# Performance work log

Measured on AMD Instinct MI355X. Metric: run time of the kernel, lower is better.

Reference implementation:

```python
import jax, jax.numpy as jnp
import numpy as np


def setup_inputs() -> dict:
    key = jax.random.key(0)
    ks = jax.random.split(key, 6)
    C, C8, W, H, B = 512, 64, 64, 64, 4
    x = jax.random.normal(ks[0], (B, C, W, H), dtype=jnp.float32)
    Wf = jax.random.normal(ks[1], (C8, C), dtype=jnp.float32) * (1.0 / np.sqrt(C))
    Wg = jax.random.normal(ks[2], (C8, C), dtype=jnp.float32) * (1.0 / np.sqrt(C))
    Wh = jax.random.normal(ks[3], (C8, C), dtype=jnp.float32) * (1.0 / np.sqrt(C))
    Wv = jax.random.normal(ks[4], (C, C8), dtype=jnp.float32) * (1.0 / np.sqrt(C8))
    gamma = jax.random.normal(ks[5], (1,), dtype=jnp.float32)
    return {"x": x, "Wf": Wf, "Wg": Wg, "Wh": Wh, "Wv": Wv, "gamma": gamma}


def reference(x, Wf, Wg, Wh, Wv, gamma):
    b, c, w, h = x.shape
    n = w * h
    xf = x.reshape(b, c, n)                       # [b, c, n]
    # 1x1 convs == channel-mixing GEMMs
    f = jnp.einsum('oc,bcn->bon', Wf, xf)         # [b, c8, n]
    g = jnp.einsum('oc,bcn->bon', Wg, xf)         # [b, c8, n]
    hmap = jnp.einsum('oc,bcn->bon', Wh, xf)      # [b, c8, n]
    # attn_map[b, i, j] = sum_c f[b, c, i] * g[b, c, j]  (f permuted as in torch)
    attn = jnp.einsum('bci,bcj->bij', f, g)       # [b, n, n]
    # unconventional softmax over dim=1 (rows / the i axis)
    attn = jax.nn.softmax(attn, axis=1)
    sa = jnp.einsum('bcn,bnj->bcj', hmap, attn)   # [b, c8, n]
    sa = sa.reshape(b, -1, w, h)                  # [b, c8, w, h]
    sa = jnp.einsum('oc,bcwh->bowh', Wv, sa)      # [b, c, w, h]
    out = sa * gamma[0] + x
    return out, sa
```

## Files before the change

### kernel.cpp

```cpp
#include <hip/hip_runtime.h>
#include <cstddef>

#define BB 4
#define CC 512
#define NN 4096

using half8  = __attribute__((ext_vector_type(8))) _Float16;
using fp16x2 = __attribute__((ext_vector_type(2))) __fp16;
using short8 = __attribute__((ext_vector_type(8))) short;
using us8    = __attribute__((ext_vector_type(8))) unsigned short;
using f32x4  = __attribute__((ext_vector_type(4))) float;

__device__ __forceinline__ unsigned short f2bf(float x) {
    unsigned int u = __float_as_uint(x);
    u += 0x7fffu + ((u >> 16) & 1u);
    return (unsigned short)(u >> 16);
}

__global__ __launch_bounds__(256) void prep_kernel(
    const float* __restrict__ Wf, const float* __restrict__ Wg,
    const float* __restrict__ Wh, const float* __restrict__ Wv,
    _Float16* __restrict__ Wc16, _Float16* __restrict__ Wv16)
{
    int idx = blockIdx.x * 256 + threadIdx.x;
    int stride = gridDim.x * 256;
    const int N1 = 192 * 512, N2 = 512 * 64;
    for (int i = idx; i < N1 + N2; i += stride) {
        if (i < N1) {
            int row = i >> 9, c = i & 511;
            const float* src = (row < 64) ? Wf : ((row < 128) ? Wg : Wh);
            float sc = (row >= 64 && row < 128) ? 1.4426950408889634f : 1.0f;
            Wc16[i] = (_Float16)(sc * src[(row & 63) * 512 + c]);
        } else {
            int k = i - N1;
            Wv16[k] = (_Float16)Wv[k];
        }
    }
}

__global__ __launch_bounds__(256) void proj_kernel(
    const float* __restrict__ x, const _Float16* __restrict__ Wc16,
    _Float16* __restrict__ Kf, _Float16* __restrict__ Qf,
    unsigned short* __restrict__ Vt)
{
    __shared__ float xsT[2][32][68];
    const int t    = threadIdx.x;
    const int w    = t >> 6;
    const int lane = t & 63;
    const int lh   = lane & 15;
    const int qd   = lane >> 4;
    const int b    = blockIdx.x >> 7;
    const int i0   = (blockIdx.x & 127) << 5;

    f32x4 acc[3][2];
    #pragma unroll
    for (int ot = 0; ot < 3; ot++)
        #pragma unroll
        for (int it = 0; it < 2; it++) { acc[ot][it][0]=0.f; acc[ot][it][1]=0.f; acc[ot][it][2]=0.f; acc[ot][it][3]=0.f; }

    const int ti8 = t & 7;
    const int tc2 = t >> 3;
    const float* xbase = x + (size_t)b*CC*NN + i0 + ti8*4;
    const _Float16* wbase = Wc16 + (size_t)(w*48 + lh)*512 + qd*8;

    float4 st0, st1;
    half8  wcur[2][3], wnxt[2][3];

#define LOADX(ck) do {                                                        \
    st0 = *(const float4*)(xbase + (size_t)((ck)*64 + tc2)*NN);               \
    st1 = *(const float4*)(xbase + (size_t)((ck)*64 + 32 + tc2)*NN);          \
} while (0)
#define STOREX(p_) do {                                                       \
    xsT[p_][ti8*4+0][tc2]    = st0.x; xsT[p_][ti8*4+1][tc2]    = st0.y;       \
    xsT[p_][ti8*4+2][tc2]    = st0.z; xsT[p_][ti8*4+3][tc2]    = st0.w;       \
    xsT[p_][ti8*4+0][32+tc2] = st1.x; xsT[p_][ti8*4+1][32+tc2] = st1.y;       \
    xsT[p_][ti8*4+2][32+tc2] = st1.z; xsT[p_][ti8*4+3][32+tc2] = st1.w;       \
} while (0)
#define LOADW(ck, WD) do {                                                    \
    _Pragma("unroll")                                                         \
    for (int ks_ = 0; ks_ < 2; ks_++)                                         \
        _Pragma("unroll")                                                     \
        for (int ot_ = 0; ot_ < 3; ot_++)                                     \
            WD[ks_][ot_] = *(const half8*)(wbase + (size_t)(ot_*16)*512 + (ck)*64 + ks_*32); \
} while (0)

    LOADX(0); STOREX(0);
    LOADW(0, wcur);
    __syncthreads();

    #pragma unroll
    for (int ck = 0; ck < 8; ck++) {
        const int p = ck & 1;
        if (ck < 7) { LOADX(ck + 1); LOADW(ck + 1, wnxt); }

        #pragma unroll
        for (int ks = 0; ks < 2; ks++) {
            half8 xf[2];
            #pragma unroll
            for (int it = 0; it < 2; it++) {
                const float* xr = &xsT[p][it*16 + lh][ks*32 + qd*8];
                f32x4 xa = *(const f32x4*)xr;
                f32x4 xb = *(const f32x4*)(xr + 4);
                union { fp16x2 h2[4]; half8 h8; } u;
                u.h2[0] = __builtin_amdgcn_cvt_pkrtz(xa[0], xa[1]);
                u.h2[1] = __builtin_amdgcn_cvt_pkrtz(xa[2], xa[3]);
                u.h2[2] = __builtin_amdgcn_cvt_pkrtz(xb[0], xb[1]);
                u.h2[3] = __builtin_amdgcn_cvt_pkrtz(xb[2], xb[3]);
                xf[it] = u.h8;
            }
            #pragma unroll
            for (int ot = 0; ot < 3; ot++)
                #pragma unroll
                for (int it = 0; it < 2; it++)
                    acc[ot][it] = __builtin_amdgcn_mfma_f32_16x16x32_f16(wcur[ks][ot], xf[it], acc[ot][it], 0, 0, 0);
        }

        if (ck < 7) {
            STOREX(p ^ 1);
            #pragma unroll
            for (int ks_ = 0; ks_ < 2; ks_++)
                #pragma unroll
                for (int ot_ = 0; ot_ < 3; ot_++)
                    wcur[ks_][ot_] = wnxt[ks_][ot_];
        }
        __syncthreads();
    }
#undef LOADX
#undef STOREX
#undef LOADW

    #pragma unroll
    for (int ot = 0; ot < 3; ot++) {
        int g16 = w*3 + ot;
        int m   = g16 >> 2;
        int obase = (g16 & 3)*16 + qd*4;
        #pragma unroll
        for (int it = 0; it < 2; it++) {
            int ig = i0 + it*16 + lh;
            #pragma unroll
            for (int r = 0; r < 4; r++) {
                float v = acc[ot][it][r];
                int ol = obase + r;
                if (m == 0)       Kf[((size_t)b*NN + ig)*64 + ol] = (_Float16)v;
                else if (m == 1)  Qf[((size_t)b*NN + ig)*64 + ol] = (_Float16)v;
                else              Vt[((size_t)b*64 + ol)*NN + ig] = f2bf(v);
            }
        }
    }
}

__global__ __launch_bounds__(256) void attn_kernel(
    const _Float16* __restrict__ Kf, const _Float16* __restrict__ Qf,
    const unsigned short* __restrict__ Vt,
    _Float16* __restrict__ Po16, float* __restrict__ Pl)
{
    __shared__ __align__(16) unsigned short Kbuf[128*64];
    __shared__ __align__(16) unsigned short Vbuf[64*128];
    __shared__ __align__(16) unsigned short Psh[4][16*64];

    const int t    = threadIdx.x;
    const int wv   = t >> 6;
    const int lane = t & 63;
    const int lh   = lane & 15;
    const int qd   = lane >> 4;

    const int B   = blockIdx.x;
    const int xcd = B & 7;
    const int rr  = B >> 3;
    const int b   = xcd >> 1;
    const int jt  = (rr & 31)*2 + (xcd & 1);
    const int s   = rr >> 5;
    const int j0  = (jt << 6) + wv*16;

    const unsigned short* Kfu = (const unsigned short*)Kf;

    half8 qf0, qf1;
    {
        const size_t qb = ((size_t)b*NN + j0 + lh)*64 + qd*8;
        qf0 = *(const half8*)(Qf + qb);
        qf1 = *(const half8*)(Qf + qb + 32);
    }

    f32x4 o_acc[4];
    float l_r[4];
    #pragma unroll
    for (int dt = 0; dt < 4; dt++) { o_acc[dt][0]=0.f; o_acc[dt][1]=0.f; o_acc[dt][2]=0.f; o_acc[dt][3]=0.f; }
    #pragma unroll
    for (int r = 0; r < 4; r++) l_r[r] = 0.f;

    const int koff = s*1024;
    const int ki = t >> 3, kc = t & 7;
    const int vd = t >> 4, vc = t & 15;

#define LOADC(ck) do {                                                        \
    size_t kg = ((size_t)b*NN + koff + (ck)*128)*64;                          \
    size_t vg = (size_t)b*64*NN + koff + (ck)*128;                            \
    _Pragma("unroll")                                                         \
    for (int r_ = 0; r_ < 4; r_++) {                                          \
        kst[r_] = *(const us8*)(Kfu + kg + (size_t)(r_*32 + ki)*64 + kc*8);   \
        vst[r_] = *(const us8*)(Vt  + vg + (size_t)(r_*16 + vd)*NN + vc*8);   \
    } } while (0)

#define STOREC() do {                                                         \
    _Pragma("unroll")                                                         \
    for (int r_ = 0; r_ < 4; r_++) {                                          \
        int i_ = r_*32 + ki;                                                  \
        int d_ = r_*16 + vd;                                                  \
        *(us8*)(&Kbuf[i_*64  + ((kc ^ (i_ & 7))*8)])  = kst[r_];              \
        *(us8*)(&Vbuf[d_*128 + ((vc ^ (d_ & 15))*8)]) = vst[r_];              \
    } } while (0)

    us8 kst[4], vst[4];
    LOADC(0);
    STOREC();
    __syncthreads();

    for (int ck = 0; ck < 8; ck++) {
        if (ck < 7) LOADC(ck + 1);

        #pragma unroll
        for (int half = 0; half < 2; half++) {
            const unsigned short* Kb = &Kbuf[half*64*64];
            const unsigned short* Vb = &Vbuf[0];

            f32x4 sc[4];
            #pragma unroll
            for (int it = 0; it < 4; it++) {
                sc[it][0]=0.f; sc[it][1]=0.f; sc[it][2]=0.f; sc[it][3]=0.f;
                const unsigned short* kr = Kb + (it*16 + lh)*64;
                half8 k0 = *(const half8*)(kr + ((qd     ^ (lh & 7))*8));
                half8 k1 = *(const half8*)(kr + (((4+qd) ^ (lh & 7))*8));
                sc[it] = __builtin_amdgcn_mfma_f32_16x16x32_f16(qf0, k0, sc[it], 0,0,0);
                sc[it] = __builtin_amdgcn_mfma_f32_16x16x32_f16(qf1, k1, sc[it], 0,0,0);
            }

            #pragma unroll
            for (int it = 0; it < 4; it++)
                #pragma unroll
                for (int r = 0; r < 4; r++) {
                    float p_ = exp2f(sc[it][r]);
                    l_r[r] += p_;
                    int i_ = it*16 + lh;
                    int j_ = qd*4 + r;
                    Psh[wv][j_*64 + (((i_>>3) ^ (j_ & 7))*8) + (i_ & 7)] = f2bf(p_);
                }
            asm volatile("s_waitcnt lgkmcnt(0)" ::: "memory");

            short8 pf0 = *(const short8*)&Psh[wv][lh*64 + ((qd     ^ (lh & 7))*8)];
            short8 pf1 = *(const short8*)&Psh[wv][lh*64 + (((4+qd) ^ (lh & 7))*8)];

            #pragma unroll
            for (int dt = 0; dt < 4; dt++) {
                const unsigned short* vr = Vb + (dt*16 + lh)*128;
                short8 v0 = *(const short8*)(vr + (((half*8 + qd    ) ^ lh)*8));
                short8 v1 = *(const short8*)(vr + (((half*8 + 4 + qd) ^ lh)*8));
                o_acc[dt] = __builtin_amdgcn_mfma_f32_16x16x32_bf16(pf0, v0, o_acc[dt], 0,0,0);
                o_acc[dt] = __builtin_amdgcn_mfma_f32_16x16x32_bf16(pf1, v1, o_acc[dt], 0,0,0);
            }
        }

        __syncthreads();
        if (ck < 7) STOREC();
        __syncthreads();
    }
#undef LOADC
#undef STOREC

    float inv[4];
    #pragma unroll
    for (int r = 0; r < 4; r++) {
        float l = l_r[r];
        #pragma unroll
        for (int off = 1; off < 16; off <<= 1)
            l += __shfl_xor(l, off);
        l_r[r] = l;
        inv[r] = 1.0f / l;
    }
    const size_t pbase = ((size_t)(s*4 + b)*NN + j0);
    #pragma unroll
    for (int dt = 0; dt < 4; dt++)
        #pragma unroll
        for (int r = 0; r < 4; r++)
            Po16[(pbase + qd*4 + r)*64 + dt*16 + lh] = (_Float16)(o_acc[dt][r] * inv[r]);
    if (lh == 0) {
        #pragma unroll
        for (int r = 0; r < 4; r++)
            Pl[pbase + qd*4 + r] = l_r[r];
    }
}

__global__ __launch_bounds__(256) void outproj_kernel(
    const _Float16* __restrict__ Po16, const float* __restrict__ Pl,
    const _Float16* __restrict__ Wv16,
    const float* __restrict__ x, const float* __restrict__ gamma,
    float* __restrict__ out1, float* __restrict__ out2)
{
    __shared__ float Osh[4][16][36];
    const int t    = threadIdx.x;
    const int w    = t >> 6;
    const int lane = t & 63;
    const int lh   = lane & 15;
    const int qd   = lane >> 4;
    const int b    = blockIdx.x >> 7;
    const int j0   = (blockIdx.x & 127) << 5;
    const float g  = gamma[0];

    half8 sb[2][2];
    #pragma unroll
    for (int jt2 = 0; jt2 < 2; jt2++) {
        const int j = j0 + jt2*16 + lh;
        float os[16];
        #pragma unroll
        for (int k = 0; k < 16; k++) os[k] = 0.f;
        float lsum = 0.f;
        #pragma unroll
        for (int s = 0; s < 4; s++) {
            size_t base = ((size_t)(s*4 + b)*NN + j);
            half8 v0 = *(const half8*)(Po16 + base*64 + qd*8);
            half8 v1 = *(const half8*)(Po16 + base*64 + qd*8 + 32);
            float l = Pl[base];
            #pragma unroll
            for (int k = 0; k < 8; k++) {
                os[k]   = fmaf(l, (float)v0[k], os[k]);
                os[8+k] = fmaf(l, (float)v1[k], os[8+k]);
            }
            lsum += l;
        }
        float inv = 1.0f / lsum;
        union { fp16x2 h2[4]; half8 h8; } u0, u1;
        #pragma unroll
        for (int k = 0; k < 4; k++) {
            u0.h2[k] = __builtin_amdgcn_cvt_pkrtz(os[2*k]*inv,   os[2*k+1]*inv);
            u1.h2[k] = __builtin_amdgcn_cvt_pkrtz(os[8+2*k]*inv, os[8+2*k+1]*inv);
        }
        sb[jt2][0] = u0.h8;
        sb[jt2][1] = u1.h8;
    }

    const int o_loc8 = lane >> 3;
    const int j4     = (lane & 7) * 4;

    #pragma unroll 2
    for (int ot8 = 0; ot8 < 8; ot8++) {
        const int ot = w*8 + ot8;
        const size_t wbase = (size_t)(ot*16 + lh)*64 + qd*8;
        half8 a0 = *(const half8*)(Wv16 + wbase);
        half8 a1 = *(const half8*)(Wv16 + wbase + 32);

        f32x4 acc[2];
        #pragma unroll
        for (int jt2 = 0; jt2 < 2; jt2++) {
            acc[jt2][0]=0.f; acc[jt2][1]=0.f; acc[jt2][2]=0.f; acc[jt2][3]=0.f;
            acc[jt2] = __builtin_amdgcn_mfma_f32_16x16x32_f16(a0, sb[jt2][0], acc[jt2], 0, 0, 0);
            acc[jt2] = __builtin_amdgcn_mfma_f32_16x16x32_f16(a1, sb[jt2][1], acc[jt2], 0, 0, 0);
        }

        #pragma unroll
        for (int jt2 = 0; jt2 < 2; jt2++)
            #pragma unroll
            for (int r = 0; r < 4; r++)
                Osh[w][qd*4 + r][jt2*16 + lh] = acc[jt2][r];
        asm volatile("s_waitcnt lgkmcnt(0)" ::: "memory");

        #pragma unroll
        for (int rr2 = 0; rr2 < 2; rr2++) {
            const int o_loc = o_loc8 + 8*rr2;
            f32x4 v = *(const f32x4*)&Osh[w][o_loc][j4];
            const int o  = ot*16 + o_loc;
            const size_t idx = ((size_t)b*CC + o)*NN + j0 + j4;
            f32x4 xv = *(const f32x4*)(x + idx);
            *(f32x4*)(out2 + idx) = v;
            f32x4 r1;
            r1[0] = fmaf(g, v[0], xv[0]); r1[1] = fmaf(g, v[1], xv[1]);
            r1[2] = fmaf(g, v[2], xv[2]); r1[3] = fmaf(g, v[3], xv[3]);
            *(f32x4*)(out1 + idx) = r1;
        }
        asm volatile("s_waitcnt lgkmcnt(0)" ::: "memory");
    }
}

extern "C" void kernel_launch(void* const* d_in, const int* in_sizes, int n_in,
                              void* d_out, int out_size, void* d_ws, size_t ws_size,
                              hipStream_t stream) {
    const float* x     = (const float*)d_in[0];
    const float* Wf    = (const float*)d_in[1];
    const float* Wg    = (const float*)d_in[2];
    const float* Wh    = (const float*)d_in[3];
    const float* Wv    = (const float*)d_in[4];
    const float* gamma = (const float*)d_in[5];

    float* out1 = (float*)d_out;
    float* out2 = out1 + (size_t)BB*CC*NN;

    const size_t BND = (size_t)BB*NN*64;
    char* wp = (char*)d_ws;
    _Float16*       Kf   = (_Float16*)wp;        wp += BND*2;
    _Float16*       Qf   = (_Float16*)wp;        wp += BND*2;
    unsigned short* Vt   = (unsigned short*)wp;  wp += BND*2;
    _Float16*       Po16 = (_Float16*)wp;        wp += BND*4*2;
    float*          Pl   = (float*)wp;           wp += (size_t)4*BB*NN*4;
    _Float16*       Wc16 = (_Float16*)wp;        wp += (size_t)192*512*2;
    _Float16*       Wv16 = (_Float16*)wp;

    prep_kernel<<<dim3(64), dim3(256), 0, stream>>>(Wf, Wg, Wh, Wv, Wc16, Wv16);
    proj_kernel<<<dim3(BB*128), dim3(256), 0, stream>>>(x, Wc16, Kf, Qf, Vt);
    attn_kernel<<<dim3(BB*256), dim3(256), 0, stream>>>(Kf, Qf, Vt, Po16, Pl);
    outproj_kernel<<<dim3(512), dim3(256), 0, stream>>>(Po16, Pl, Wv16, x, gamma, out1, out2);
}
```

Baseline: 173.5 us.

## Rewrite attention with 32x32 MFMA, register-resident P, async LDS loads

The attention kernel moves from 16x16x32 to 32x32x16 MFMA tiles, with 128 query columns per block and 32 per wave. The probability tile is converted to bf16 and rearranged in registers with permlane32 swaps instead of a round trip through shared memory. K and V chunks are staged with global_load_lds into double-buffered LDS, which drops the register staging and one barrier per chunk. The key-split count becomes a template parameter and uses 8 when the workspace allows, at the cost of more partial outputs for the output projection to merge.

```diff
diff --git a/kernel.cpp b/kernel.cpp
--- a/kernel.cpp
+++ b/kernel.cpp
@@ -10,6 +10,7 @@
 using short8 = __attribute__((ext_vector_type(8))) short;
 using us8    = __attribute__((ext_vector_type(8))) unsigned short;
 using f32x4  = __attribute__((ext_vector_type(4))) float;
+using f32x16 = __attribute__((ext_vector_type(16))) float;
 
 __device__ __forceinline__ unsigned short f2bf(float x) {
     unsigned int u = __float_as_uint(x);
@@ -149,146 +150,142 @@
     }
 }
 
-__global__ __launch_bounds__(256) void attn_kernel(
+template<int SPLITS>
+__global__ __launch_bounds__(256, 3) void attn_kernel(
     const _Float16* __restrict__ Kf, const _Float16* __restrict__ Qf,
     const unsigned short* __restrict__ Vt,
     _Float16* __restrict__ Po16, float* __restrict__ Pl)
 {
-    __shared__ __align__(16) unsigned short Kbuf[128*64];
-    __shared__ __align__(16) unsigned short Vbuf[64*128];
-    __shared__ __align__(16) unsigned short Psh[4][16*64];
+    static_assert(NN % SPLITS == 0, "split");
+    constexpr int KS  = NN / SPLITS;
+    constexpr int NCH = KS / 64;
+
+    __shared__ __align__(16) unsigned short Kb2[2][64*64];
+    __shared__ __align__(16) unsigned short Vb2[2][64*64];
 
     const int t    = threadIdx.x;
     const int wv   = t >> 6;
     const int lane = t & 63;
-    const int lh   = lane & 15;
-    const int qd   = lane >> 4;
-
-    const int B   = blockIdx.x;
-    const int xcd = B & 7;
-    const int rr  = B >> 3;
-    const int b   = xcd >> 1;
-    const int jt  = (rr & 31)*2 + (xcd & 1);
-    const int s   = rr >> 5;
-    const int j0  = (jt << 6) + wv*16;
-
-    const unsigned short* Kfu = (const unsigned short*)Kf;
-
-    half8 qf0, qf1;
+    const int il   = lane & 31;
+    const int h    = lane >> 5;
+
+    const int p  = blockIdx.x;
+    const int v  = (p & 7) * (SPLITS * 16) + (p >> 3);
+    const int jt = v & 31;
+    const int bs = v >> 5;
+    const int b  = bs / SPLITS;
+    const int s  = bs % SPLITS;
+    const int j0w  = jt*128 + wv*32;
+    const int koff = s * KS;
+
+    half8 qfr[4];
     {
-        const size_t qb = ((size_t)b*NN + j0 + lh)*64 + qd*8;
-        qf0 = *(const half8*)(Qf + qb);
-        qf1 = *(const half8*)(Qf + qb + 32);
-    }
-
-    f32x4 o_acc[4];
-    float l_r[4];
-    #pragma unroll
-    for (int dt = 0; dt < 4; dt++) { o_acc[dt][0]=0.f; o_acc[dt][1]=0.f; o_acc[dt][2]=0.f; o_acc[dt][3]=0.f; }
-    #pragma unroll
-    for (int r = 0; r < 4; r++) l_r[r] = 0.f;
-
-    const int koff = s*1024;
-    const int ki = t >> 3, kc = t & 7;
-    const int vd = t >> 4, vc = t & 15;
-
-#define LOADC(ck) do {                                                        \
-    size_t kg = ((size_t)b*NN + koff + (ck)*128)*64;                          \
-    size_t vg = (size_t)b*64*NN + koff + (ck)*128;                            \
-    _Pragma("unroll")                                                         \
-    for (int r_ = 0; r_ < 4; r_++) {                                          \
-        kst[r_] = *(const us8*)(Kfu + kg + (size_t)(r_*32 + ki)*64 + kc*8);   \
-        vst[r_] = *(const us8*)(Vt  + vg + (size_t)(r_*16 + vd)*NN + vc*8);   \
+        const _Float16* qp = Qf + ((size_t)b*NN + j0w + il)*64 + h*8;
+        #pragma unroll
+        for (int sl = 0; sl < 4; sl++) qfr[sl] = *(const half8*)(qp + sl*16);
+    }
+
+    f32x16 o_acc[2];
+    #pragma unroll
+    for (int dt = 0; dt < 2; dt++)
+        #pragma unroll
+        for (int r = 0; r < 16; r++) o_acc[dt][r] = 0.f;
+    float l4[4] = {0.f, 0.f, 0.f, 0.f};
+
+#define STAGE(ck, pb) do {                                                          \
+    const size_t bi_ = (size_t)koff + (size_t)(ck)*64;                              \
+    _Pragma("unroll")                                                               \
+    for (int r_ = 0; r_ < 2; r_++) {                                                \
+        const int slot_ = r_*256 + t;                                               \
+        const int ik_ = slot_ >> 3, c8_ = slot_ & 7;                                \
+        const int sw_ = (c8_ ^ (ik_ & 7)) << 3;                                     \
+        const _Float16* gk_ = Kf + ((size_t)b*NN + bi_ + ik_)*64 + sw_;             \
+        __builtin_amdgcn_global_load_lds(                                           \
+            (const __attribute__((address_space(1))) void*)gk_,                     \
+            (__attribute__((address_space(3))) void*)&Kb2[pb][(r_*256 + wv*64)*8],  \
+            16, 0, 0);                                                              \
+        const unsigned short* gv_ = Vt + ((size_t)b*64 + ik_)*NN + bi_ + sw_;       \
+        __builtin_amdgcn_global_load_lds(                                           \
+            (const __attribute__((address_space(1))) void*)gv_,                     \
+            (__attribute__((address_space(3))) void*)&Vb2[pb][(r_*256 + wv*64)*8],  \
+            16, 0, 0);                                                              \
     } } while (0)
 
-#define STOREC() do {                                                         \
-    _Pragma("unroll")                                                         \
-    for (int r_ = 0; r_ < 4; r_++) {                                          \
-        int i_ = r_*32 + ki;                                                  \
-        int d_ = r_*16 + vd;                                                  \
-        *(us8*)(&Kbuf[i_*64  + ((kc ^ (i_ & 7))*8)])  = kst[r_];              \
-        *(us8*)(&Vbuf[d_*128 + ((vc ^ (d_ & 15))*8)]) = vst[r_];              \
-    } } while (0)
-
-    us8 kst[4], vst[4];
-    LOADC(0);
-    STOREC();
+    STAGE(0, 0);
     __syncthreads();
 
-    for (int ck = 0; ck < 8; ck++) {
-        if (ck < 7) LOADC(ck + 1);
-
-        #pragma unroll
-        for (int half = 0; half < 2; half++) {
-            const unsigned short* Kb = &Kbuf[half*64*64];
-            const unsigned short* Vb = &Vbuf[0];
-
-            f32x4 sc[4];
-            #pragma unroll
-            for (int it = 0; it < 4; it++) {
-                sc[it][0]=0.f; sc[it][1]=0.f; sc[it][2]=0.f; sc[it][3]=0.f;
-                const unsigned short* kr = Kb + (it*16 + lh)*64;
-                half8 k0 = *(const half8*)(kr + ((qd     ^ (lh & 7))*8));
-                half8 k1 = *(const half8*)(kr + (((4+qd) ^ (lh & 7))*8));
-                sc[it] = __builtin_amdgcn_mfma_f32_16x16x32_f16(qf0, k0, sc[it], 0,0,0);
-                sc[it] = __builtin_amdgcn_mfma_f32_16x16x32_f16(qf1, k1, sc[it], 0,0,0);
+    for (int ck = 0; ck < NCH; ck++) {
+        const int cb = ck & 1;
+        if (ck + 1 < NCH) STAGE(ck + 1, cb ^ 1);
+
+        const unsigned short* Kb = Kb2[cb];
+        const unsigned short* Vb = Vb2[cb];
+
+        #pragma unroll
+        for (int isub = 0; isub < 2; isub++) {
+            const int irow = isub*32 + il;
+            const unsigned short* kr = Kb + irow*64;
+            f32x16 sc;
+            #pragma unroll
+            for (int r = 0; r < 16; r++) sc[r] = 0.f;
+            #pragma unroll
+            for (int sl = 0; sl < 4; sl++) {
+                half8 kf = *(const half8*)(kr + (((sl*2 + h) ^ (irow & 7)) << 3));
+                sc = __builtin_amdgcn_mfma_f32_32x32x16_f16(kf, qfr[sl], sc, 0, 0, 0);
             }
 
-            #pragma unroll
-            for (int it = 0; it < 4; it++)
+            float pq[16];
+            #pragma unroll
+            for (int r = 0; r < 16; r++) pq[r] = exp2f(sc[r]);
+            #pragma unroll
+            for (int r = 0; r < 16; r++) l4[r & 3] += pq[r];
+
+            unsigned wA[8];
+            #pragma unroll
+            for (int k = 0; k < 8; k++)
+                asm("v_cvt_pk_bf16_f32 %0, %1, %2" : "=v"(wA[k]) : "v"(pq[2*k]), "v"(pq[2*k+1]));
+            asm("v_permlane32_swap_b32 %0, %1" : "+v"(wA[0]), "+v"(wA[2]));
+            asm("v_permlane32_swap_b32 %0, %1" : "+v"(wA[1]), "+v"(wA[3]));
+            asm("v_permlane32_swap_b32 %0, %1" : "+v"(wA[4]), "+v"(wA[6]));
+            asm("v_permlane32_swap_b32 %0, %1" : "+v"(wA[5]), "+v"(wA[7]));
+
+            union { unsigned u[4]; short8 s8; } pa0, pa1;
+            pa0.u[0]=wA[0]; pa0.u[1]=wA[1]; pa0.u[2]=wA[2]; pa0.u[3]=wA[3];
+            pa1.u[0]=wA[4]; pa1.u[1]=wA[5]; pa1.u[2]=wA[6]; pa1.u[3]=wA[7];
+
+            #pragma unroll
+            for (int isl = 0; isl < 2; isl++) {
+                const short8 paf = isl ? pa1.s8 : pa0.s8;
+                const int vc = isub*4 + isl*2 + h;
                 #pragma unroll
-                for (int r = 0; r < 4; r++) {
-                    float p_ = exp2f(sc[it][r]);
-                    l_r[r] += p_;
-                    int i_ = it*16 + lh;
-                    int j_ = qd*4 + r;
-                    Psh[wv][j_*64 + (((i_>>3) ^ (j_ & 7))*8) + (i_ & 7)] = f2bf(p_);
+                for (int dt = 0; dt < 2; dt++) {
+                    const int drow = dt*32 + il;
+                    short8 vf = *(const short8*)(Vb + drow*64 + ((vc ^ (drow & 7)) << 3));
+                    o_acc[dt] = __builtin_amdgcn_mfma_f32_32x32x16_bf16(paf, vf, o_acc[dt], 0, 0, 0);
                 }
-            asm volatile("s_waitcnt lgkmcnt(0)" ::: "memory");
-
-            short8 pf0 = *(const short8*)&Psh[wv][lh*64 + ((qd     ^ (lh & 7))*8)];
-            short8 pf1 = *(const short8*)&Psh[wv][lh*64 + (((4+qd) ^ (lh & 7))*8)];
-
-            #pragma unroll
-            for (int dt = 0; dt < 4; dt++) {
-                const unsigned short* vr = Vb + (dt*16 + lh)*128;
-                short8 v0 = *(const short8*)(vr + (((half*8 + qd    ) ^ lh)*8));
-                short8 v1 = *(const short8*)(vr + (((half*8 + 4 + qd) ^ lh)*8));
-                o_acc[dt] = __builtin_amdgcn_mfma_f32_16x16x32_bf16(pf0, v0, o_acc[dt], 0,0,0);
-                o_acc[dt] = __builtin_amdgcn_mfma_f32_16x16x32_bf16(pf1, v1, o_acc[dt], 0,0,0);
             }
         }
-
         __syncthreads();
-        if (ck < 7) STOREC();
-        __syncthreads();
-    }
-#undef LOADC
-#undef STOREC
-
-    float inv[4];
-    #pragma unroll
-    for (int r = 0; r < 4; r++) {
-        float l = l_r[r];
-        #pragma unroll
-        for (int off = 1; off < 16; off <<= 1)
-            l += __shfl_xor(l, off);
-        l_r[r] = l;
-        inv[r] = 1.0f / l;
-    }
-    const size_t pbase = ((size_t)(s*4 + b)*NN + j0);
-    #pragma unroll
-    for (int dt = 0; dt < 4; dt++)
-        #pragma unroll
-        for (int r = 0; r < 4; r++)
-            Po16[(pbase + qd*4 + r)*64 + dt*16 + lh] = (_Float16)(o_acc[dt][r] * inv[r]);
-    if (lh == 0) {
-        #pragma unroll
-        for (int r = 0; r < 4; r++)
-            Pl[pbase + qd*4 + r] = l_r[r];
-    }
-}
-
+    }
+#undef STAGE
+
+    float l_acc  = (l4[0] + l4[1]) + (l4[2] + l4[3]);
+    float l_full = l_acc + __shfl_xor(l_acc, 32);
+    float inv = 1.0f / l_full;
+
+    const size_t pbase = (size_t)(s*4 + b)*NN + j0w;
+    #pragma unroll
+    for (int r = 0; r < 16; r++) {
+        const int jr = (r & 3) + 8*(r >> 2) + 4*h;
+        const float invr = __shfl(inv, jr);
+        #pragma unroll
+        for (int dt = 0; dt < 2; dt++)
+            Po16[(pbase + jr)*64 + dt*32 + il] = (_Float16)(o_acc[dt][r] * invr);
+    }
+    if (h == 0) Pl[pbase + il] = l_full;
+}
+
+template<int SPLITS>
 __global__ __launch_bounds__(256) void outproj_kernel(
     const _Float16* __restrict__ Po16, const float* __restrict__ Pl,
     const _Float16* __restrict__ Wv16,
@@ -314,7 +311,7 @@
         for (int k = 0; k < 16; k++) os[k] = 0.f;
         float lsum = 0.f;
         #pragma unroll
-        for (int s = 0; s < 4; s++) {
+        for (int s = 0; s < SPLITS; s++) {
             size_t base = ((size_t)(s*4 + b)*NN + j);
             half8 v0 = *(const half8*)(Po16 + base*64 + qd*8);
             half8 v1 = *(const half8*)(Po16 + base*64 + qd*8 + 32);
@@ -393,17 +390,26 @@
     float* out2 = out1 + (size_t)BB*CC*NN;
 
     const size_t BND = (size_t)BB*NN*64;
+    const size_t need8 = BND*2*3 + BND*2*8 + (size_t)8*BB*NN*4
+                       + (size_t)192*512*2 + (size_t)512*64*2;
+    const int SPL = (ws_size >= need8) ? 8 : 4;
+
     char* wp = (char*)d_ws;
     _Float16*       Kf   = (_Float16*)wp;        wp += BND*2;
     _Float16*       Qf   = (_Float16*)wp;        wp += BND*2;
     unsigned short* Vt   = (unsigned short*)wp;  wp += BND*2;
-    _Float16*       Po16 = (_Float16*)wp;        wp += BND*4*2;
-    float*          Pl   = (float*)wp;           wp += (size_t)4*BB*NN*4;
+    _Float16*       Po16 = (_Float16*)wp;        wp += BND*2*SPL;
+    float*          Pl   = (float*)wp;           wp += (size_t)SPL*BB*NN*4;
     _Float16*       Wc16 = (_Float16*)wp;        wp += (size_t)192*512*2;
     _Float16*       Wv16 = (_Float16*)wp;
 
     prep_kernel<<<dim3(64), dim3(256), 0, stream>>>(Wf, Wg, Wh, Wv, Wc16, Wv16);
     proj_kernel<<<dim3(BB*128), dim3(256), 0, stream>>>(x, Wc16, Kf, Qf, Vt);
-    attn_kernel<<<dim3(BB*256), dim3(256), 0, stream>>>(Kf, Qf, Vt, Po16, Pl);
-    outproj_kernel<<<dim3(512), dim3(256), 0, stream>>>(Po16, Pl, Wv16, x, gamma, out1, out2);
-}
+    if (SPL == 8) {
+        attn_kernel<8><<<dim3(128*8), dim3(256), 0, stream>>>(Kf, Qf, Vt, Po16, Pl);
+        outproj_kernel<8><<<dim3(512), dim3(256), 0, stream>>>(Po16, Pl, Wv16, x, gamma, out1, out2);
+    } else {
+        attn_kernel<4><<<dim3(128*4), dim3(256), 0, stream>>>(Kf, Qf, Vt, Po16, Pl);
+        outproj_kernel<4><<<dim3(512), dim3(256), 0, stream>>>(Po16, Pl, Wv16, x, gamma, out1, out2);
+    }
+}
```

Measured after the change: 164.3 us. -5.3%, faster.
